# Performance work log

Hardware: AMD Instinct MI355X
Metric: run time of the kernel (lower is better)

## Reference

```python
import jax, jax.numpy as jnp
import numpy as np

TOP_K = 2
NORM_TOPK_PROB = True


def setup_inputs() -> dict:
    key = jax.random.key(0)
    k1, k2, k3 = jax.random.split(key, 3)
    B, S, H, E = 4, 2048, 2048, 8
    hidden_states = jax.random.normal(k1, (B, S, H), dtype=jnp.float32)
    gate_w = jax.random.normal(k2, (E, H), dtype=jnp.float32) * 0.02   # nn.Linear weight [E, H]
    expert_w = jax.random.normal(k3, (E, H, H), dtype=jnp.float32) * 0.02  # per-expert Linear weight [H_out, H_in]
    return {"hidden_states": hidden_states, "gate_w": gate_w, "expert_w": expert_w}


def reference(hidden_states, gate_w, expert_w):
    B, S, H = hidden_states.shape
    E = gate_w.shape[0]
    x = hidden_states.reshape(-1, H)                      # [T, H], T = B*S
    T = x.shape[0]

    router_logits = x @ gate_w.T                          # [T, E]
    probs = jax.nn.softmax(router_logits.astype(jnp.float32), axis=-1)
    top_w, top_i = jax.lax.top_k(probs, TOP_K)            # [T, K]
    if NORM_TOPK_PROB:
        top_w = top_w / jnp.sum(top_w, axis=-1, keepdims=True)
    top_w = top_w.astype(x.dtype)

    # dense [T, E] combine weights (scatter of top-k weights)
    w_full = jnp.zeros((T, E), dtype=x.dtype).at[jnp.arange(T)[:, None], top_i].add(top_w)

    # expert_i(x) = x @ W_i.T  (bias-free Linear)
    expert_out = jnp.einsum('th,eoh->eto', x, expert_w)   # [E, T, H]
    out = jnp.einsum('te,eto->to', w_full, expert_out)    # [T, H]

    return out.reshape(B, S, H), router_logits.reshape(B, S, E)
```

## Files before the change

### kernel.cpp

```cpp
#include <hip/hip_runtime.h>
#include <stdint.h>

#define T_TOK 8192
#define HDIM  2048
#define NEXP  8
#define TILE  128
#define BK    64
#define RTOK  32

typedef __bf16 bf16x8 __attribute__((ext_vector_type(8)));
typedef float  f32x4  __attribute__((ext_vector_type(4)));
typedef unsigned short u16;
typedef u16    u16x8  __attribute__((ext_vector_type(8)));

typedef const __attribute__((address_space(1))) void* gptr_t;
typedef __attribute__((address_space(3))) void* lptr_t;

static __device__ __forceinline__ u16 f2bf(float f) {
    union { float f; unsigned u; } v; v.f = f;
    unsigned u = v.u;
    u = (u + 0x7FFFu + ((u >> 16) & 1u)) >> 16;
    return (u16)u;
}

__global__ __launch_bounds__(256) void cvt_kernel(const float* __restrict__ in,
                                                  u16* __restrict__ out, int n8) {
    int i = blockIdx.x * 256 + threadIdx.x;
    if (i >= n8) return;
    const float4* p = (const float4*)in + (size_t)i * 2;
    float4 a = p[0], b = p[1];
    u16x8 r;
    r[0] = f2bf(a.x); r[1] = f2bf(a.y); r[2] = f2bf(a.z); r[3] = f2bf(a.w);
    r[4] = f2bf(b.x); r[5] = f2bf(b.y); r[6] = f2bf(b.z); r[7] = f2bf(b.w);
    ((u16x8*)out)[i] = r;
}

__global__ __launch_bounds__(256) void router_kernel(const float* __restrict__ x,
                                                     const float* __restrict__ gw,
                                                     u16* __restrict__ xb,
                                                     float* __restrict__ logits_out,
                                                     int* __restrict__ cnt,
                                                     int* __restrict__ rows,
                                                     float* __restrict__ wts) {
    __shared__ int   lcnt[NEXP];
    __shared__ int   lbase[NEXP];
    __shared__ int   lrows[NEXP][RTOK];
    __shared__ float lwtsS[NEXP][RTOK];

    int tid  = threadIdx.x;
    int lane = tid & 63;
    int wave = tid >> 6;
    if (tid < NEXP) lcnt[tid] = 0;
    __syncthreads();

    int t0 = blockIdx.x * RTOK + wave * 8;
    const float4* g4 = (const float4*)gw;

    float acc[8][NEXP] = {};
    #pragma unroll
    for (int i = 0; i < HDIM / 4 / 64; i++) {
        int idx = lane + i * 64;
        float4 gv[NEXP];
        #pragma unroll
        for (int e = 0; e < NEXP; e++) gv[e] = g4[e * (HDIM / 4) + idx];
        #pragma unroll
        for (int tk = 0; tk < 8; tk++) {
            int t = t0 + tk;
            float4 xv = ((const float4*)(x + (size_t)t * HDIM))[idx];
            ushort4 h;
            h.x = f2bf(xv.x); h.y = f2bf(xv.y); h.z = f2bf(xv.z); h.w = f2bf(xv.w);
            ((ushort4*)(xb + (size_t)t * HDIM))[idx] = h;
            #pragma unroll
            for (int e = 0; e < NEXP; e++)
                acc[tk][e] += xv.x * gv[e].x + xv.y * gv[e].y +
                              xv.z * gv[e].z + xv.w * gv[e].w;
        }
    }
    #pragma unroll
    for (int tk = 0; tk < 8; tk++)
        #pragma unroll
        for (int e = 0; e < NEXP; e++)
            #pragma unroll
            for (int off = 32; off > 0; off >>= 1)
                acc[tk][e] += __shfl_xor(acc[tk][e], off, 64);

    if (lane == 0) {
        #pragma unroll
        for (int tk = 0; tk < 8; tk++) {
            int t = t0 + tk;
            #pragma unroll
            for (int e = 0; e < NEXP; e++) logits_out[(size_t)t * NEXP + e] = acc[tk][e];
            int e0 = 0;
            #pragma unroll
            for (int e = 1; e < NEXP; e++) if (acc[tk][e] > acc[tk][e0]) e0 = e;
            int e1 = (e0 == 0) ? 1 : 0;
            #pragma unroll
            for (int e = 0; e < NEXP; e++)
                if (e != e0 && acc[tk][e] > acc[tk][e1]) e1 = e;
            float w0 = 1.0f / (1.0f + expf(acc[tk][e1] - acc[tk][e0]));
            int p0 = atomicAdd(&lcnt[e0], 1);
            lrows[e0][p0] = t; lwtsS[e0][p0] = w0;
            int p1 = atomicAdd(&lcnt[e1], 1);
            lrows[e1][p1] = t; lwtsS[e1][p1] = 1.0f - w0;
        }
    }
    __syncthreads();
    if (tid < NEXP) lbase[tid] = atomicAdd(&cnt[tid], lcnt[tid]);
    __syncthreads();
    int e = tid >> 5, j = tid & 31;
    if (j < lcnt[e]) {
        int b = lbase[e] + j;
        rows[e * T_TOK + b] = lrows[e][j];
        wts[e * T_TOK + b]  = lwtsS[e][j];
    }
}

__global__ __launch_bounds__(256) void moe_gemm(const u16* __restrict__ xb,
                                                const u16* __restrict__ wb,
                                                const int* __restrict__ cnt,
                                                const int* __restrict__ rows,
                                                const float* __restrict__ wts,
                                                float* __restrict__ out) {
    int p  = blockIdx.x;
    int xc = p & 7;
    int q  = p >> 3;
    int rt = q & 63;
    int g  = (q >> 6) * 8 + xc;
    int e  = g >> 4;
    int nb = (g & 15) * TILE;

    int count = cnt[e];
    int rowBase = rt * TILE;
    if (rowBase >= count) return;

    const u16*   W     = wb  + (size_t)e * HDIM * HDIM;
    const int*   rlist = rows + e * T_TOK;
    const float* wlist = wts  + e * T_TOK;

    __shared__ u16 As[TILE * BK];
    __shared__ u16 Bs[TILE * BK];

    int tid  = threadIdx.x;
    int lane = tid & 63;
    int wave = tid >> 6;
    int wr = wave >> 1, wc = wave & 1;

    const u16* a_src[4];
    const u16* b_src[4];
    #pragma unroll
    for (int pp = 0; pp < 4; pp++) {
        int row  = (tid >> 3) + pp * 32;
        int clog = (tid & 7) ^ (row & 7);
        int tok  = rlist[min(rowBase + row, count - 1)];
        a_src[pp] = xb + (size_t)tok * HDIM + clog * 8;
        b_src[pp] = W + (size_t)(nb + row) * HDIM + clog * 8;
    }
    int wslot = (tid & ~63);
    u16* lds_a[4]; u16* lds_b[4];
    #pragma unroll
    for (int pp = 0; pp < 4; pp++) {
        lds_a[pp] = As + (size_t)(pp * 256 + wslot) * 8;
        lds_b[pp] = Bs + (size_t)(pp * 256 + wslot) * 8;
    }

    int lrow = lane & 15;
    int kq   = lane >> 4;
    int mloc[4], nloc[4];
    #pragma unroll
    for (int i = 0; i < 4; i++) {
        mloc[i] = wr * 64 + i * 16 + lrow;
        nloc[i] = wc * 64 + i * 16 + lrow;
    }

    f32x4 acc[4][4] = {};

    for (int kb = 0; kb < HDIM; kb += BK) {
        __syncthreads();
        #pragma unroll
        for (int pp = 0; pp < 4; pp++) {
            __builtin_amdgcn_global_load_lds((gptr_t)(a_src[pp] + kb),
                                             (lptr_t)lds_a[pp], 16, 0, 0);
            __builtin_amdgcn_global_load_lds((gptr_t)(b_src[pp] + kb),
                                             (lptr_t)lds_b[pp], 16, 0, 0);
        }
        __syncthreads();

        #pragma unroll
        for (int s = 0; s < 2; s++) {
            int chunk = s * 4 + kq;
            bf16x8 a[4], b[4];
            #pragma unroll
            for (int i = 0; i < 4; i++) {
                int aslot = (mloc[i] << 3) | (chunk ^ (mloc[i] & 7));
                int bslot = (nloc[i] << 3) | (chunk ^ (nloc[i] & 7));
                a[i] = *(const bf16x8*)(As + aslot * 8);
                b[i] = *(const bf16x8*)(Bs + bslot * 8);
            }
            #pragma unroll
            for (int mt = 0; mt < 4; mt++)
                #pragma unroll
                for (int nt = 0; nt < 4; nt++)
                    acc[mt][nt] = __builtin_amdgcn_mfma_f32_16x16x32_bf16(
                                      a[mt], b[nt], acc[mt][nt], 0, 0, 0);
        }
    }

    int srow = (lane >> 4) * 4;
    #pragma unroll
    for (int mt = 0; mt < 4; mt++) {
        #pragma unroll
        for (int r = 0; r < 4; r++) {
            int row = rowBase + wr * 64 + mt * 16 + srow + r;
            if (row < count) {
                int   tok = rlist[row];
                float wgt = wlist[row];
                #pragma unroll
                for (int nt = 0; nt < 4; nt++) {
                    int col = nb + wc * 64 + nt * 16 + lrow;
                    atomicAdd(out + (size_t)tok * HDIM + col, wgt * acc[mt][nt][r]);
                }
            }
        }
    }
}

extern "C" void kernel_launch(void* const* d_in, const int* in_sizes, int n_in,
                              void* d_out, int out_size, void* d_ws, size_t ws_size,
                              hipStream_t stream) {
    const float* x  = (const float*)d_in[0];
    const float* gw = (const float*)d_in[1];
    const float* ew = (const float*)d_in[2];
    float* out    = (float*)d_out;
    float* logits = out + (size_t)T_TOK * HDIM;

    char* ws = (char*)d_ws;
    int*   cnt  = (int*)ws;
    int*   rows = (int*)(ws + 1024);
    float* wts  = (float*)(ws + 1024 + 262144);
    u16*   xb   = (u16*)(ws + 1024 + 2 * 262144);
    u16*   wb   = xb + (size_t)T_TOK * HDIM;

    hipMemsetAsync(d_out, 0, (size_t)T_TOK * HDIM * sizeof(float), stream);
    hipMemsetAsync(cnt, 0, NEXP * sizeof(int), stream);

    int nw8 = NEXP * HDIM * HDIM / 8;
    cvt_kernel<<<(nw8 + 255) / 256, 256, 0, stream>>>(ew, wb, nw8);

    router_kernel<<<T_TOK / RTOK, 256, 0, stream>>>(x, gw, xb, logits, cnt, rows, wts);

    moe_gemm<<<NEXP * 64 * 16, 256, 0, stream>>>(xb, wb, cnt, rows, wts, out);
}
```

Before: 643.5 us.

## Double-buffer LDS tiles to overlap global loads with MFMA compute

Splits the A and B shared-memory tiles into two buffers and restructures the K loop into a ping-pong schedule. The next tile's async global-to-LDS loads are issued before the current tile's MFMA work, and there is one barrier per stage instead of two. The goal is to hide global memory latency behind compute. In exchange, LDS use per block doubles, which may lower the number of resident blocks per CU.

Result: slower. 659.2 us (+2.4%).

```diff
diff --git a/kernel.cpp b/kernel.cpp
--- a/kernel.cpp
+++ b/kernel.cpp
@@ -137,8 +137,8 @@
     const int*   rlist = rows + e * T_TOK;
     const float* wlist = wts  + e * T_TOK;
 
-    __shared__ u16 As[TILE * BK];
-    __shared__ u16 Bs[TILE * BK];
+    __shared__ u16 As[2][TILE * BK];
+    __shared__ u16 Bs[2][TILE * BK];
 
     int tid  = threadIdx.x;
     int lane = tid & 63;
@@ -156,12 +156,18 @@
         b_src[pp] = W + (size_t)(nb + row) * HDIM + clog * 8;
     }
     int wslot = (tid & ~63);
-    u16* lds_a[4]; u16* lds_b[4];
-    #pragma unroll
-    for (int pp = 0; pp < 4; pp++) {
-        lds_a[pp] = As + (size_t)(pp * 256 + wslot) * 8;
-        lds_b[pp] = Bs + (size_t)(pp * 256 + wslot) * 8;
-    }
+
+    auto stage = [&](u16* A_lds, u16* B_lds, int kb) {
+        #pragma unroll
+        for (int pp = 0; pp < 4; pp++) {
+            __builtin_amdgcn_global_load_lds((gptr_t)(a_src[pp] + kb),
+                                             (lptr_t)(A_lds + (pp * 256 + wslot) * 8),
+                                             16, 0, 0);
+            __builtin_amdgcn_global_load_lds((gptr_t)(b_src[pp] + kb),
+                                             (lptr_t)(B_lds + (pp * 256 + wslot) * 8),
+                                             16, 0, 0);
+        }
+    };
 
     int lrow = lane & 15;
     int kq   = lane >> 4;
@@ -174,17 +180,7 @@
 
     f32x4 acc[4][4] = {};
 
-    for (int kb = 0; kb < HDIM; kb += BK) {
-        __syncthreads();
-        #pragma unroll
-        for (int pp = 0; pp < 4; pp++) {
-            __builtin_amdgcn_global_load_lds((gptr_t)(a_src[pp] + kb),
-                                             (lptr_t)lds_a[pp], 16, 0, 0);
-            __builtin_amdgcn_global_load_lds((gptr_t)(b_src[pp] + kb),
-                                             (lptr_t)lds_b[pp], 16, 0, 0);
-        }
-        __syncthreads();
-
+    auto compute = [&](const u16* A_lds, const u16* B_lds) {
         #pragma unroll
         for (int s = 0; s < 2; s++) {
             int chunk = s * 4 + kq;
@@ -193,8 +189,8 @@
             for (int i = 0; i < 4; i++) {
                 int aslot = (mloc[i] << 3) | (chunk ^ (mloc[i] & 7));
                 int bslot = (nloc[i] << 3) | (chunk ^ (nloc[i] & 7));
-                a[i] = *(const bf16x8*)(As + aslot * 8);
-                b[i] = *(const bf16x8*)(Bs + bslot * 8);
+                a[i] = *(const bf16x8*)(A_lds + aslot * 8);
+                b[i] = *(const bf16x8*)(B_lds + bslot * 8);
             }
             #pragma unroll
             for (int mt = 0; mt < 4; mt++)
@@ -203,6 +199,17 @@
                     acc[mt][nt] = __builtin_amdgcn_mfma_f32_16x16x32_bf16(
                                       a[mt], b[nt], acc[mt][nt], 0, 0, 0);
         }
+    };
+
+    stage(As[0], Bs[0], 0);
+    __syncthreads();
+    for (int kb = 0; kb < HDIM - BK; kb += 2 * BK) {
+        stage(As[1], Bs[1], kb + BK);
+        compute(As[0], Bs[0]);
+        __syncthreads();
+        if (kb + 2 * BK < HDIM) stage(As[0], Bs[0], kb + 2 * BK);
+        compute(As[1], Bs[1]);
+        __syncthreads();
     }
 
     int srow = (lane >> 4) * 4;
```
